# Performance work log

Hardware: AMD Instinct MI355X
Metric: run time of the kernel (lower is better)

Reference implementation:

```python
import jax, jax.numpy as jnp
import numpy as np
import math

B, S, D, H, DFF = 2, 2048, 1024, 16, 4096
DK = D // H
EPS = 1e-5


def setup_inputs() -> dict:
    key = jax.random.key(0)
    ks = jax.random.split(key, 8)
    s = 0.02
    return {
        "x": jax.random.normal(ks[0], (B, S, D), jnp.float32),
        "src_mask": jnp.ones((B, 1, 1, S), jnp.int32),
        "wq": jax.random.normal(ks[1], (D, D), jnp.float32) * s,
        "bq": jnp.zeros((D,), jnp.float32),
        "wk": jax.random.normal(ks[2], (D, D), jnp.float32) * s,
        "bk": jnp.zeros((D,), jnp.float32),
        "wv": jax.random.normal(ks[3], (D, D), jnp.float32) * s,
        "bv": jnp.zeros((D,), jnp.float32),
        "wo": jax.random.normal(ks[4], (D, D), jnp.float32) * s,
        "bo": jnp.zeros((D,), jnp.float32),
        "w1": jax.random.normal(ks[5], (DFF, D), jnp.float32) * s,
        "b1": jnp.zeros((DFF,), jnp.float32),
        "w2": jax.random.normal(ks[6], (D, DFF), jnp.float32) * s,
        "b2": jnp.zeros((D,), jnp.float32),
        "alpha1": jnp.ones((1,), jnp.float32),
        "bias1": jnp.ones((1,), jnp.float32),
        "alpha2": jnp.ones((1,), jnp.float32),
        "bias2": jnp.ones((1,), jnp.float32),
    }


def _layernorm(x, alpha, bias):
    # Faithful to source: unbiased std (ddof=1), divide by (std + eps),
    # scalar alpha/bias both initialized to 1.
    mean = jnp.mean(x, axis=-1, keepdims=True)
    std = jnp.std(x, axis=-1, keepdims=True, ddof=1)
    return alpha * (x - mean) / (std + EPS) + bias


def _mha(x, wq, bq, wk, bk, wv, bv, wo, bo):
    q = (x @ wq.T + bq).reshape(B, S, H, DK).swapaxes(1, 2)  # b h s d
    k = (x @ wk.T + bk).reshape(B, S, H, DK).swapaxes(1, 2)
    v = (x @ wv.T + bv).reshape(B, S, H, DK).swapaxes(1, 2)
    scores = jnp.einsum("bhqd,bhkd->bhqk", q, k) / math.sqrt(DK)
    # NOTE: source calls masked_fill (out-of-place) and discards the result,
    # so the mask has NO effect. Reproduced faithfully: no masking here.
    attn = jax.nn.softmax(scores, axis=-1)
    out = jnp.einsum("bhqk,bhkd->bhqd", attn, v)
    out = out.swapaxes(1, 2).reshape(B, S, D)
    return out @ wo.T + bo


def reference(x, src_mask, wq, bq, wk, bk, wv, bv, wo, bo,
              w1, b1, w2, b2, alpha1, bias1, alpha2, bias2):
    # residual[0]: x + attn(norm(x)) (dropout=0 -> identity)
    h1 = x + _mha(_layernorm(x, alpha1, bias1), wq, bq, wk, bk, wv, bv, wo, bo)
    # residual[1]: h1 + ffn(norm(h1))
    n2 = _layernorm(h1, alpha2, bias2)
    ffn = (n2 @ w1.T + b1) @ w2.T + b2
    return h1 + ffn
```

## Files before the change

### kernel.cpp

```cpp
#include <hip/hip_runtime.h>
#include <stdint.h>

#define Bx   2
#define Sx   2048
#define Dx   1024
#define Hx   16
#define DKx  64
#define DFFx 4096
#define Mx   4096

#define CEXP 0.18033688011112042f

typedef __attribute__((ext_vector_type(8))) short short8;
typedef __attribute__((ext_vector_type(4))) float f32x4;
typedef __attribute__((ext_vector_type(4))) unsigned short ushort4v;

__device__ __forceinline__ unsigned short f2b(float f) {
    union { float f; uint32_t u; } v; v.f = f;
    uint32_t u = v.u;
    u += 0x7fffu + ((u >> 16) & 1u);
    return (unsigned short)(u >> 16);
}

__device__ __forceinline__ float fexp2(float x) {
#if __has_builtin(__builtin_amdgcn_exp2f)
    return __builtin_amdgcn_exp2f(x);
#else
    return exp2f(x);
#endif
}

__global__ __launch_bounds__(256) void conv_all(
    const float4* __restrict__ wq, const float4* __restrict__ wk,
    const float4* __restrict__ wv, const float4* __restrict__ wo,
    const float4* __restrict__ w1, const float4* __restrict__ w2,
    const float4* __restrict__ bq, const float4* __restrict__ bk,
    const float4* __restrict__ bv,
    ushort4v* __restrict__ dqkv, ushort4v* __restrict__ dwo,
    ushort4v* __restrict__ d1, ushort4v* __restrict__ d2,
    float4* __restrict__ dbias) {
    const int i = blockIdx.x * 256 + threadIdx.x;
    const int S4 = 1 << 18;
    if (i < 4 * S4) {
        const float4* s; ushort4v* d;
        if (i < S4)          { s = wq + i;            d = dqkv + i; }
        else if (i < 2 * S4) { s = wk + (i - S4);     d = dqkv + i; }
        else if (i < 3 * S4) { s = wv + (i - 2 * S4); d = dqkv + i; }
        else                 { s = wo + (i - 3 * S4); d = dwo + (i - 3 * S4); }
        const float4 v = *s;
        ushort4v o; o.x = f2b(v.x); o.y = f2b(v.y); o.z = f2b(v.z); o.w = f2b(v.w);
        *d = o;
    } else if (i < 8 * S4) {
        const float4 v = w1[i - 4 * S4];
        ushort4v o; o.x = f2b(v.x); o.y = f2b(v.y); o.z = f2b(v.z); o.w = f2b(v.w);
        d1[i - 4 * S4] = o;
    } else if (i < 12 * S4) {
        const float4 v = w2[i - 8 * S4];
        ushort4v o; o.x = f2b(v.x); o.y = f2b(v.y); o.z = f2b(v.z); o.w = f2b(v.w);
        d2[i - 8 * S4] = o;
    } else if (i < 12 * S4 + 768) {
        const int jn = i - 12 * S4;
        dbias[jn] = (jn < 256) ? bq[jn] : (jn < 512 ? bk[jn - 256] : bv[jn - 512]);
    }
}

__global__ __launch_bounds__(256) void layernorm_k(const float* __restrict__ x,
                                                   const float* __restrict__ alpha,
                                                   const float* __restrict__ beta,
                                                   unsigned short* __restrict__ out) {
    __shared__ float red[8];
    const int row = blockIdx.x;
    const int t = threadIdx.x, lane = t & 63, w = t >> 6;
    float4 v = ((const float4*)(x + (size_t)row * Dx))[t];
    float s = v.x + v.y + v.z + v.w;
    float q = v.x*v.x + v.y*v.y + v.z*v.z + v.w*v.w;
#pragma unroll
    for (int off = 1; off < 64; off <<= 1) {
        s += __shfl_xor(s, off);
        q += __shfl_xor(q, off);
    }
    if (lane == 0) { red[w] = s; red[4 + w] = q; }
    __syncthreads();
    s = red[0] + red[1] + red[2] + red[3];
    q = red[4] + red[5] + red[6] + red[7];
    const float mean = s * (1.0f / Dx);
    float var = (q - (float)Dx * mean * mean) * (1.0f / (Dx - 1));
    var = fmaxf(var, 0.0f);
    const float inv = alpha[0] / (sqrtf(var) + 1e-5f);
    const float bb = beta[0];
    ushort4v o;
    o.x = f2b((v.x - mean) * inv + bb);
    o.y = f2b((v.y - mean) * inv + bb);
    o.z = f2b((v.z - mean) * inv + bb);
    o.w = f2b((v.w - mean) * inv + bb);
    *(ushort4v*)(out + (size_t)row * Dx + t * 4) = o;
}

#define GLDS(gp, lp) __builtin_amdgcn_global_load_lds( \
    (const __attribute__((address_space(1))) unsigned int*)(gp), \
    (__attribute__((address_space(3))) unsigned int*)(lp), 16, 0, 0)

#define STAGE(buf, kt) do {                                                     \
    const int k0_ = (kt) << 5;                                                  \
    _Pragma("unroll")                                                           \
    for (int i_ = 0; i_ < MB/2; ++i_) {                                         \
      const int ca_ = (MB==4) ? (w*2 + i_) : w;                                 \
      GLDS(A + (size_t)(bm + ca_*16 + srow)*K + k0_ + skc*8, &As[buf][ca_*512]);\
    }                                                                           \
    _Pragma("unroll")                                                           \
    for (int i_ = 0; i_ < 2; ++i_) {                                            \
      const int cb_ = w*2 + i_;                                                 \
      GLDS(W + (size_t)(bn + cb_*16 + srow)*K + k0_ + skc*8, &Bs[buf][cb_*512]);\
    }                                                                           \
  } while (0)

template<int BM>
__global__ __launch_bounds__(256) void gemm2(const short* __restrict__ A,
                                             const short* __restrict__ W,
                                             const float* __restrict__ bias,
                                             const float* __restrict__ res,
                                             float* __restrict__ Cout,
                                             int M, int N, int K) {
    constexpr int MB = BM / 32;
    __shared__ alignas(16) short As[2][BM * 32];
    __shared__ alignas(16) short Bs[2][128 * 32];
    const int t = threadIdx.x, lane = t & 63, w = t >> 6;
    const int bb = blockIdx.x, xcd = bb & 7, jj = bb >> 3;
    const int bn = (jj & 7) * 128;
    const int bm = (xcd * 8 + (jj >> 3)) * BM;
    const int wm = (w >> 1) * (BM / 2), wn = (w & 1) * 64;
    const int srow = lane >> 2, skc = lane & 3;

    f32x4 acc[MB][4] = {};
    const int nkt = K >> 5;

    STAGE(0, 0);
    __syncthreads();
    int cur = 0;
    for (int kt = 0; kt < nkt; ++kt) {
        if (kt + 1 < nkt) STAGE(cur ^ 1, kt + 1);
        const short* as = &As[cur][0];
        const short* bs = &Bs[cur][0];
        short8 af[MB], bfr[4];
#pragma unroll
        for (int mb = 0; mb < MB; ++mb)
            af[mb] = *(const short8*)&as[(wm + mb * 16 + (lane & 15)) * 32 + (lane >> 4) * 8];
#pragma unroll
        for (int nb = 0; nb < 4; ++nb)
            bfr[nb] = *(const short8*)&bs[(wn + nb * 16 + (lane & 15)) * 32 + (lane >> 4) * 8];
#pragma unroll
        for (int mb = 0; mb < MB; ++mb)
#pragma unroll
            for (int nb = 0; nb < 4; ++nb)
                acc[mb][nb] = __builtin_amdgcn_mfma_f32_16x16x32_bf16(af[mb], bfr[nb], acc[mb][nb], 0, 0, 0);
        __syncthreads();
        cur ^= 1;
    }

    const int r0 = (lane >> 4) * 4, c0 = lane & 15;
#pragma unroll
    for (int mb = 0; mb < MB; ++mb)
#pragma unroll
        for (int nb = 0; nb < 4; ++nb) {
            const int col = bn + wn + nb * 16 + c0;
            const float bv = bias[col];
            const int row0 = bm + wm + mb * 16 + r0;
#pragma unroll
            for (int r = 0; r < 4; ++r) {
                const size_t idx = (size_t)(row0 + r) * N + col;
                Cout[idx] = acc[mb][nb][r] + bv + res[idx];
            }
        }
}

template<int MODE>
__global__ __launch_bounds__(256) void gemm128(const short* __restrict__ A,
                                               const short* __restrict__ W,
                                               const float* __restrict__ bias,
                                               void* __restrict__ Cout,
                                               int N, int K,
                                               unsigned short* __restrict__ Qout,
                                               unsigned short* __restrict__ Kout,
                                               unsigned short* __restrict__ Vout) {
    constexpr int MB = 4;
    __shared__ alignas(16) short As[2][128 * 32];
    __shared__ alignas(16) short Bs[2][128 * 32];
    const int t = threadIdx.x, lane = t & 63, w = t >> 6;
    const int bb = blockIdx.x, bpx = gridDim.x >> 3;
    const int g = (bb & 7) * bpx + (bb >> 3);
    const int bn = (g >> 5) * 128;
    const int bm = (g & 31) * 128;
    const int wm = (w >> 1) * 64, wn = (w & 1) * 64;
    const int srow = lane >> 2, skc = lane & 3;

    f32x4 acc[MB][4] = {};
    const int nkt = K >> 5;

    STAGE(0, 0);
    __syncthreads();
    int cur = 0;
    for (int kt = 0; kt < nkt; ++kt) {
        if (kt + 1 < nkt) STAGE(cur ^ 1, kt + 1);
        const short* as = &As[cur][0];
        const short* bs = &Bs[cur][0];
        short8 af[MB], bfr[4];
#pragma unroll
        for (int mb = 0; mb < MB; ++mb)
            af[mb] = *(const short8*)&as[(wm + mb * 16 + (lane & 15)) * 32 + (lane >> 4) * 8];
#pragma unroll
        for (int nb = 0; nb < 4; ++nb)
            bfr[nb] = *(const short8*)&bs[(wn + nb * 16 + (lane & 15)) * 32 + (lane >> 4) * 8];
#pragma unroll
        for (int mb = 0; mb < MB; ++mb)
#pragma unroll
            for (int nb = 0; nb < 4; ++nb)
                acc[mb][nb] = __builtin_amdgcn_mfma_f32_16x16x32_bf16(af[mb], bfr[nb], acc[mb][nb], 0, 0, 0);
        __syncthreads();
        cur ^= 1;
    }

    const int r0 = (lane >> 4) * 4, c0 = lane & 15;
#pragma unroll
    for (int mb = 0; mb < MB; ++mb)
#pragma unroll
        for (int nb = 0; nb < 4; ++nb) {
            const int col = bn + wn + nb * 16 + c0;
            const float bv = bias[col];
            const int row0 = bm + wm + mb * 16 + r0;
            if (MODE == 0) {
#pragma unroll
                for (int r = 0; r < 4; ++r)
                    ((unsigned short*)Cout)[(size_t)(row0 + r) * N + col] = f2b(acc[mb][nb][r] + bv);
            } else {
                if (col < 1024) {
#pragma unroll
                    for (int r = 0; r < 4; ++r)
                        Qout[(size_t)(row0 + r) * 1024 + col] = f2b((acc[mb][nb][r] + bv) * CEXP);
                } else if (col < 2048) {
#pragma unroll
                    for (int r = 0; r < 4; ++r)
                        Kout[(size_t)(row0 + r) * 1024 + (col - 1024)] = f2b(acc[mb][nb][r] + bv);
                } else {
                    const int dk = col - 2048, hh = dk >> 6, dlo = dk & 63;
                    const int bbv = row0 >> 11, s0 = row0 & 2047;
                    const int vrow = (bbv * 16 + hh) * 64 + dlo;
                    ushort4v pv;
                    pv.x = f2b(acc[mb][nb][0] + bv);
                    pv.y = f2b(acc[mb][nb][1] + bv);
                    pv.z = f2b(acc[mb][nb][2] + bv);
                    pv.w = f2b(acc[mb][nb][3] + bv);
                    *(ushort4v*)&Vout[(size_t)vrow * Sx + s0] = pv;
                }
            }
        }
}

__global__ __launch_bounds__(256) void gemmsk(const short* __restrict__ A,
                                              const short* __restrict__ W,
                                              float* __restrict__ P0,
                                              float* __restrict__ P1,
                                              int K) {
    constexpr int MB = 4;
    __shared__ alignas(16) short As[2][128 * 32];
    __shared__ alignas(16) short Bs[2][128 * 32];
    const int t = threadIdx.x, lane = t & 63, w = t >> 6;
    const int bb = blockIdx.x, xcd = bb & 7, jj = bb >> 3;
    const int bn = (jj & 7) * 128;
    const int p = (xcd << 3) | (jj >> 3);
    const int bm = (p & 31) * 128;
    const int kz = p >> 5;
    float* __restrict__ P = kz ? P1 : P0;
    const int wm = (w >> 1) * 64, wn = (w & 1) * 64;
    const int srow = lane >> 2, skc = lane & 3;

    f32x4 acc[MB][4] = {};
    const int nkt = (K >> 1) >> 5;
    const int kbeg = kz * nkt;

    STAGE(0, kbeg);
    __syncthreads();
    int cur = 0;
    for (int kt = kbeg; kt < kbeg + nkt; ++kt) {
        if (kt + 1 < kbeg + nkt) STAGE(cur ^ 1, kt + 1);
        const short* as = &As[cur][0];
        const short* bs = &Bs[cur][0];
        short8 af[MB], bfr[4];
#pragma unroll
        for (int mb = 0; mb < MB; ++mb)
            af[mb] = *(const short8*)&as[(wm + mb * 16 + (lane & 15)) * 32 + (lane >> 4) * 8];
#pragma unroll
        for (int nb = 0; nb < 4; ++nb)
            bfr[nb] = *(const short8*)&bs[(wn + nb * 16 + (lane & 15)) * 32 + (lane >> 4) * 8];
#pragma unroll
        for (int mb = 0; mb < MB; ++mb)
#pragma unroll
            for (int nb = 0; nb < 4; ++nb)
                acc[mb][nb] = __builtin_amdgcn_mfma_f32_16x16x32_bf16(af[mb], bfr[nb], acc[mb][nb], 0, 0, 0);
        __syncthreads();
        cur ^= 1;
    }

    const int r0 = (lane >> 4) * 4, c0 = lane & 15;
#pragma unroll
    for (int mb = 0; mb < MB; ++mb)
#pragma unroll
        for (int nb = 0; nb < 4; ++nb) {
            const int col = bn + wn + nb * 16 + c0;
            const int row0 = bm + wm + mb * 16 + r0;
#pragma unroll
            for (int r = 0; r < 4; ++r)
                P[(size_t)(row0 + r) * Dx + col] = acc[mb][nb][r];
        }
}

__global__ __launch_bounds__(256) void epi2(const float4* __restrict__ p0,
                                            const float4* __restrict__ p1,
                                            const float4* __restrict__ b2,
                                            const float4* __restrict__ h1,
                                            float4* __restrict__ out) {
    const int i = blockIdx.x * 256 + threadIdx.x;
    const float4 bv = b2[i & 255];
    const float4 a = p0[i], b = p1[i], h = h1[i];
    float4 o;
    o.x = a.x + b.x + h.x + bv.x;
    o.y = a.y + b.y + h.y + bv.y;
    o.z = a.z + b.z + h.z + bv.z;
    o.w = a.w + b.w + h.w + bv.w;
    out[i] = o;
}

__global__ __launch_bounds__(256) void attn_fwd6(const short* __restrict__ Q,
                                                 const short* __restrict__ Kg,
                                                 const short* __restrict__ Vtg,
                                                 unsigned short* __restrict__ O) {
    __shared__ alignas(16) short Ks[2][64 * 64];
    __shared__ alignas(16) short Vs[2][64 * 64];
    __shared__ alignas(16) short Pl[4][32 * 64];
    const int t = threadIdx.x, lane = t & 63, w = t >> 6;
    const int bh = blockIdx.x;
    const int b = bh >> 4, h = bh & 15;
    const int q0 = blockIdx.y * 128 + w * 32;
    const int lo = lane & 15, hi = lane >> 4;

    short8 qf[2][2];
#pragma unroll
    for (int mb = 0; mb < 2; ++mb)
#pragma unroll
        for (int kf = 0; kf < 2; ++kf)
            qf[mb][kf] = *(const short8*)&Q[(size_t)(b * Sx + q0 + mb * 16 + lo) * Dx
                                            + h * DKx + kf * 32 + hi * 8];

    f32x4 o_[2][4] = {};
    f32x4 l_acc[2] = {};
    short8 ones;
#pragma unroll
    for (int j = 0; j < 8; ++j) ones[j] = (short)0x3F80;

    const int srow = t >> 2;
    const int scol2 = (t & 3) * 32;
    const int swz = (srow & 7) << 4;
    const short* Kbase = Kg + (size_t)(b * Sx) * Dx + h * DKx;
    const short* Vbase = Vtg + (size_t)(bh * 64 + srow) * Sx;
    char* PwB = (char*)&Pl[w][0];

    short8 kr0, kr1, vr0, vr1;
    {
        const short* kp = Kbase + (size_t)srow * Dx + (t & 3) * 16;
        kr0 = *(const short8*)kp; kr1 = *(const short8*)(kp + 8);
        const short* vp = Vbase + (t & 3) * 16;
        vr0 = *(const short8*)vp; vr1 = *(const short8*)(vp + 8);
        char* KsB = (char*)&Ks[0][0];
        char* VsB = (char*)&Vs[0][0];
        *(short8*)(KsB + ((srow * 128 + scol2) ^ swz)) = kr0;
        *(short8*)(KsB + ((srow * 128 + scol2 + 16) ^ swz)) = kr1;
        *(short8*)(VsB + ((srow * 128 + scol2) ^ swz)) = vr0;
        *(short8*)(VsB + ((srow * 128 + scol2 + 16) ^ swz)) = vr1;
    }
    __syncthreads();

    int cur = 0;
    for (int kt = 0; kt < Sx / 64; ++kt) {
        const bool more = (kt + 1 < Sx / 64);
        if (more) {
            const short* kp = Kbase + (size_t)((kt + 1) * 64 + srow) * Dx + (t & 3) * 16;
            kr0 = *(const short8*)kp; kr1 = *(const short8*)(kp + 8);
            const short* vp = Vbase + (kt + 1) * 64 + (t & 3) * 16;
            vr0 = *(const short8*)vp; vr1 = *(const short8*)(vp + 8);
        }
        char* KsB = (char*)&Ks[cur][0];
        char* VsB = (char*)&Vs[cur][0];

        f32x4 s[2][4] = {};
        __builtin_amdgcn_s_setprio(1);
#pragma unroll
        for (int nb = 0; nb < 4; ++nb) {
            const int key = nb * 16 + lo;
            const int ksw = (key & 7) << 4;
#pragma unroll
            for (int kf = 0; kf < 2; ++kf) {
                const short8 kfr = *(const short8*)(KsB + ((key * 128 + kf * 64 + hi * 16) ^ ksw));
#pragma unroll
                for (int mb = 0; mb < 2; ++mb)
                    s[mb][nb] = __builtin_amdgcn_mfma_f32_16x16x32_bf16(qf[mb][kf], kfr, s[mb][nb], 0, 0, 0);
            }
        }
        __builtin_amdgcn_s_setprio(0);

#pragma unroll
        for (int mb = 0; mb < 2; ++mb)
#pragma unroll
            for (int nb = 0; nb < 4; ++nb) {
                const int k = nb * 16 + lo;
#pragma unroll
                for (int r = 0; r < 4; ++r) {
                    const float p = fexp2(s[mb][nb][r]);
                    union { float f; uint32_t u; } cv; cv.f = p;
                    const int qq = mb * 16 + hi * 4 + r;
                    *(short*)(PwB + ((qq * 128 + k * 2) ^ ((qq & 7) << 4))) = (short)(cv.u >> 16);
                }
            }

        short8 pa[2][2];
#pragma unroll
        for (int mb = 0; mb < 2; ++mb)
#pragma unroll
            for (int kc = 0; kc < 2; ++kc)
                pa[mb][kc] = *(const short8*)(PwB + (((mb * 16 + lo) * 128 + kc * 64 + hi * 16) ^ ((lo & 7) << 4)));

        __builtin_amdgcn_s_setprio(1);
#pragma unroll
        for (int mb = 0; mb < 2; ++mb) {
            l_acc[mb] = __builtin_amdgcn_mfma_f32_16x16x32_bf16(pa[mb][0], ones, l_acc[mb], 0, 0, 0);
            l_acc[mb] = __builtin_amdgcn_mfma_f32_16x16x32_bf16(pa[mb][1], ones, l_acc[mb], 0, 0, 0);
        }

#pragma unroll
        for (int d = 0; d < 4; ++d) {
            const int vd = d * 16 + lo;
            const int vsw = (vd & 7) << 4;
#pragma unroll
            for (int kc = 0; kc < 2; ++kc) {
                const short8 vf = *(const short8*)(VsB + ((vd * 128 + kc * 64 + hi * 16) ^ vsw));
#pragma unroll
                for (int mb = 0; mb < 2; ++mb)
                    o_[mb][d] = __builtin_amdgcn_mfma_f32_16x16x32_bf16(pa[mb][kc], vf, o_[mb][d], 0, 0, 0);
            }
        }
        __builtin_amdgcn_s_setprio(0);

        if (more) {
            char* KsN = (char*)&Ks[cur ^ 1][0];
            char* VsN = (char*)&Vs[cur ^ 1][0];
            *(short8*)(KsN + ((srow * 128 + scol2) ^ swz)) = kr0;
            *(short8*)(KsN + ((srow * 128 + scol2 + 16) ^ swz)) = kr1;
            *(short8*)(VsN + ((srow * 128 + scol2) ^ swz)) = vr0;
            *(short8*)(VsN + ((srow * 128 + scol2 + 16) ^ swz)) = vr1;
        }
        __syncthreads();
        cur ^= 1;
    }

#pragma unroll
    for (int mb = 0; mb < 2; ++mb)
#pragma unroll
        for (int d = 0; d < 4; ++d)
#pragma unroll
            for (int r = 0; r < 4; ++r) {
                const int qrow = b * Sx + q0 + mb * 16 + hi * 4 + r;
                O[(size_t)qrow * Dx + h * DKx + d * 16 + lo] = f2b(o_[mb][d][r] / l_acc[mb][r]);
            }
}

extern "C" void kernel_launch(void* const* d_in, const int* in_sizes, int n_in,
                              void* d_out, int out_size, void* d_ws, size_t ws_size,
                              hipStream_t stream) {
    const float* x  = (const float*)d_in[0];
    const float* wq = (const float*)d_in[2];
    const float* bq = (const float*)d_in[3];
    const float* wk = (const float*)d_in[4];
    const float* bk = (const float*)d_in[5];
    const float* wv = (const float*)d_in[6];
    const float* bv = (const float*)d_in[7];
    const float* wo = (const float*)d_in[8];
    const float* bo = (const float*)d_in[9];
    const float* w1 = (const float*)d_in[10];
    const float* b1 = (const float*)d_in[11];
    const float* w2 = (const float*)d_in[12];
    const float* b2 = (const float*)d_in[13];
    const float* alpha1 = (const float*)d_in[14];
    const float* bias1  = (const float*)d_in[15];
    const float* alpha2 = (const float*)d_in[16];
    const float* bias2  = (const float*)d_in[17];
    float* out = (float*)d_out;

    short* ws   = (short*)d_ws;
    short* wqkv = ws;
    short* wob  = wqkv + 3145728;
    short* w1b  = wob  + 1048576;
    short* w2b  = w1b  + 4194304;
    short* n1   = w2b  + 4194304;
    short* Qb   = n1   + 4194304;
    short* Kb   = Qb   + 4194304;
    short* Vt   = Kb   + 4194304;
    short* f1   = Vt   + 4194304;
    float* h1   = (float*)(f1 + 16777216);
    float* bqkv = (float*)((char*)h1 + ((size_t)Mx * Dx * 4));
    short* ao = n1;
    short* n2 = n1;
    float* p0 = (float*)n1;
    float* p1 = (float*)Kb;

    conv_all<<<12291, 256, 0, stream>>>((const float4*)wq, (const float4*)wk,
                                        (const float4*)wv, (const float4*)wo,
                                        (const float4*)w1, (const float4*)w2,
                                        (const float4*)bq, (const float4*)bk,
                                        (const float4*)bv,
                                        (ushort4v*)wqkv, (ushort4v*)wob,
                                        (ushort4v*)w1b, (ushort4v*)w2b,
                                        (float4*)bqkv);

    layernorm_k<<<Mx, 256, 0, stream>>>(x, alpha1, bias1, (unsigned short*)n1);

    gemm128<2><<<768, 256, 0, stream>>>(n1, wqkv, bqkv, nullptr, 3072, Dx,
                                        (unsigned short*)Qb, (unsigned short*)Kb,
                                        (unsigned short*)Vt);

    attn_fwd6<<<dim3(32, 16), 256, 0, stream>>>(Qb, Kb, Vt, (unsigned short*)ao);

    gemm2<64><<<512, 256, 0, stream>>>(ao, wob, bo, x, h1, Mx, Dx, Dx);

    layernorm_k<<<Mx, 256, 0, stream>>>(h1, alpha2, bias2, (unsigned short*)n2);

    gemm128<0><<<1024, 256, 0, stream>>>(n2, w1b, b1, f1, DFFx, Dx,
                                         nullptr, nullptr, nullptr);

    gemmsk<<<512, 256, 0, stream>>>(f1, w2b, p0, p1, DFFx);
    epi2<<<4096, 256, 0, stream>>>((const float4*)p0, (const float4*)p1,
                                   (const float4*)b2, (const float4*)h1, (float4*)out);
}
```

Baseline: 361.6 us.

## Use 256x256 tiles with 512 threads for QKV and FFN1 GEMMs, transpose MFMA operands

Replaces the 128x128 gemm128 kernel with a gemm256 kernel that computes 256x256 output tiles using 8 waves, which doubles operand reuse per LDS load and lowers global traffic per FLOP. Across all GEMMs the MFMA operand order is swapped so each lane holds four consecutive columns, which allows vectorized float4/ushort4 epilogue stores. The trade-offs are higher register pressure (32 accumulators per wave) and fewer blocks (192/256) on the device. The V-transpose output also goes from one packed store to four scalar stores.

```diff
diff --git a/kernel.cpp b/kernel.cpp
--- a/kernel.cpp
+++ b/kernel.cpp
@@ -125,6 +125,7 @@
     __shared__ alignas(16) short As[2][BM * 32];
     __shared__ alignas(16) short Bs[2][128 * 32];
     const int t = threadIdx.x, lane = t & 63, w = t >> 6;
+    const int lo = lane & 15, hi = lane >> 4;
     const int bb = blockIdx.x, xcd = bb & 7, jj = bb >> 3;
     const int bn = (jj & 7) * 128;
     const int bm = (xcd * 8 + (jj >> 3)) * BM;
@@ -144,112 +145,136 @@
         short8 af[MB], bfr[4];
 #pragma unroll
         for (int mb = 0; mb < MB; ++mb)
-            af[mb] = *(const short8*)&as[(wm + mb * 16 + (lane & 15)) * 32 + (lane >> 4) * 8];
+            af[mb] = *(const short8*)&as[(wm + mb * 16 + lo) * 32 + hi * 8];
 #pragma unroll
         for (int nb = 0; nb < 4; ++nb)
-            bfr[nb] = *(const short8*)&bs[(wn + nb * 16 + (lane & 15)) * 32 + (lane >> 4) * 8];
+            bfr[nb] = *(const short8*)&bs[(wn + nb * 16 + lo) * 32 + hi * 8];
 #pragma unroll
         for (int mb = 0; mb < MB; ++mb)
 #pragma unroll
             for (int nb = 0; nb < 4; ++nb)
-                acc[mb][nb] = __builtin_amdgcn_mfma_f32_16x16x32_bf16(af[mb], bfr[nb], acc[mb][nb], 0, 0, 0);
+                acc[mb][nb] = __builtin_amdgcn_mfma_f32_16x16x32_bf16(bfr[nb], af[mb], acc[mb][nb], 0, 0, 0);
         __syncthreads();
         cur ^= 1;
     }
 
-    const int r0 = (lane >> 4) * 4, c0 = lane & 15;
 #pragma unroll
     for (int mb = 0; mb < MB; ++mb)
 #pragma unroll
         for (int nb = 0; nb < 4; ++nb) {
-            const int col = bn + wn + nb * 16 + c0;
-            const float bv = bias[col];
-            const int row0 = bm + wm + mb * 16 + r0;
-#pragma unroll
-            for (int r = 0; r < 4; ++r) {
-                const size_t idx = (size_t)(row0 + r) * N + col;
-                Cout[idx] = acc[mb][nb][r] + bv + res[idx];
-            }
-        }
-}
+            const int row = bm + wm + mb * 16 + lo;
+            const int col0 = bn + wn + nb * 16 + hi * 4;
+            const float4 bv4 = *(const float4*)&bias[col0];
+            const size_t idx = (size_t)row * N + col0;
+            const float4 rs4 = *(const float4*)&res[idx];
+            float4 o4;
+            o4.x = acc[mb][nb][0] + bv4.x + rs4.x;
+            o4.y = acc[mb][nb][1] + bv4.y + rs4.y;
+            o4.z = acc[mb][nb][2] + bv4.z + rs4.z;
+            o4.w = acc[mb][nb][3] + bv4.w + rs4.w;
+            *(float4*)&Cout[idx] = o4;
+        }
+}
+
+#define STG256(buf, kt) do {                                                     \
+    const int k0_ = (kt) << 5;                                                   \
+    _Pragma("unroll")                                                            \
+    for (int i_ = 0; i_ < 2; ++i_) {                                             \
+      const int c_ = i_ * 8 + w;                                                 \
+      GLDS(A + (size_t)(bm + c_*16 + (lane>>2))*K + k0_ + (lane&3)*8,            \
+           &As[buf][c_*512]);                                                    \
+      GLDS(W + (size_t)(bn + c_*16 + (lane>>2))*K + k0_ + (lane&3)*8,            \
+           &Bs[buf][c_*512]);                                                    \
+    }                                                                            \
+  } while (0)
 
 template<int MODE>
-__global__ __launch_bounds__(256) void gemm128(const short* __restrict__ A,
-                                               const short* __restrict__ W,
-                                               const float* __restrict__ bias,
-                                               void* __restrict__ Cout,
-                                               int N, int K,
-                                               unsigned short* __restrict__ Qout,
-                                               unsigned short* __restrict__ Kout,
-                                               unsigned short* __restrict__ Vout) {
-    constexpr int MB = 4;
-    __shared__ alignas(16) short As[2][128 * 32];
-    __shared__ alignas(16) short Bs[2][128 * 32];
+__global__ __launch_bounds__(512, 2) void gemm256(const short* __restrict__ A,
+                                                  const short* __restrict__ W,
+                                                  const float* __restrict__ bias,
+                                                  void* __restrict__ Cout,
+                                                  int M, int N, int K,
+                                                  int nbn, int rpx,
+                                                  unsigned short* __restrict__ Qout,
+                                                  unsigned short* __restrict__ Kout,
+                                                  unsigned short* __restrict__ Vout) {
+    __shared__ alignas(16) short As[2][256 * 32];
+    __shared__ alignas(16) short Bs[2][256 * 32];
     const int t = threadIdx.x, lane = t & 63, w = t >> 6;
-    const int bb = blockIdx.x, bpx = gridDim.x >> 3;
-    const int g = (bb & 7) * bpx + (bb >> 3);
-    const int bn = (g >> 5) * 128;
-    const int bm = (g & 31) * 128;
-    const int wm = (w >> 1) * 64, wn = (w & 1) * 64;
-    const int srow = lane >> 2, skc = lane & 3;
-
-    f32x4 acc[MB][4] = {};
+    const int lo = lane & 15, hi = lane >> 4;
+    const int bb = blockIdx.x, xcd = bb & 7, jj = bb >> 3;
+    const int bm = (xcd * rpx + jj / nbn) * 256;
+    const int bn = (jj % nbn) * 256;
+    const int wr = w >> 2, wc = w & 3;
+
+    f32x4 acc[8][4] = {};
     const int nkt = K >> 5;
 
-    STAGE(0, 0);
+    STG256(0, 0);
     __syncthreads();
     int cur = 0;
     for (int kt = 0; kt < nkt; ++kt) {
-        if (kt + 1 < nkt) STAGE(cur ^ 1, kt + 1);
+        if (kt + 1 < nkt) STG256(cur ^ 1, kt + 1);
         const short* as = &As[cur][0];
         const short* bs = &Bs[cur][0];
-        short8 af[MB], bfr[4];
-#pragma unroll
-        for (int mb = 0; mb < MB; ++mb)
-            af[mb] = *(const short8*)&as[(wm + mb * 16 + (lane & 15)) * 32 + (lane >> 4) * 8];
+        short8 bfr[4];
 #pragma unroll
         for (int nb = 0; nb < 4; ++nb)
-            bfr[nb] = *(const short8*)&bs[(wn + nb * 16 + (lane & 15)) * 32 + (lane >> 4) * 8];
-#pragma unroll
-        for (int mb = 0; mb < MB; ++mb)
-#pragma unroll
-            for (int nb = 0; nb < 4; ++nb)
-                acc[mb][nb] = __builtin_amdgcn_mfma_f32_16x16x32_bf16(af[mb], bfr[nb], acc[mb][nb], 0, 0, 0);
+            bfr[nb] = *(const short8*)&bs[(wc * 64 + nb * 16 + lo) * 32 + hi * 8];
+#pragma unroll
+        for (int mh = 0; mh < 2; ++mh) {
+            short8 af[4];
+#pragma unroll
+            for (int mb = 0; mb < 4; ++mb)
+                af[mb] = *(const short8*)&as[(wr * 128 + mh * 64 + mb * 16 + lo) * 32 + hi * 8];
+#pragma unroll
+            for (int mb = 0; mb < 4; ++mb)
+#pragma unroll
+                for (int nb = 0; nb < 4; ++nb)
+                    acc[mh * 4 + mb][nb] =
+                        __builtin_amdgcn_mfma_f32_16x16x32_bf16(bfr[nb], af[mb], acc[mh * 4 + mb][nb], 0, 0, 0);
+        }
         __syncthreads();
         cur ^= 1;
     }
 
-    const int r0 = (lane >> 4) * 4, c0 = lane & 15;
-#pragma unroll
-    for (int mb = 0; mb < MB; ++mb)
+#pragma unroll
+    for (int mb = 0; mb < 8; ++mb)
 #pragma unroll
         for (int nb = 0; nb < 4; ++nb) {
-            const int col = bn + wn + nb * 16 + c0;
-            const float bv = bias[col];
-            const int row0 = bm + wm + mb * 16 + r0;
+            const int row = bm + wr * 128 + mb * 16 + lo;
+            const int col0 = bn + wc * 64 + nb * 16 + hi * 4;
+            const float4 bv4 = *(const float4*)&bias[col0];
             if (MODE == 0) {
-#pragma unroll
-                for (int r = 0; r < 4; ++r)
-                    ((unsigned short*)Cout)[(size_t)(row0 + r) * N + col] = f2b(acc[mb][nb][r] + bv);
+                ushort4v pv;
+                pv.x = f2b(acc[mb][nb][0] + bv4.x);
+                pv.y = f2b(acc[mb][nb][1] + bv4.y);
+                pv.z = f2b(acc[mb][nb][2] + bv4.z);
+                pv.w = f2b(acc[mb][nb][3] + bv4.w);
+                *(ushort4v*)&((unsigned short*)Cout)[(size_t)row * N + col0] = pv;
             } else {
-                if (col < 1024) {
-#pragma unroll
-                    for (int r = 0; r < 4; ++r)
-                        Qout[(size_t)(row0 + r) * 1024 + col] = f2b((acc[mb][nb][r] + bv) * CEXP);
-                } else if (col < 2048) {
-#pragma unroll
-                    for (int r = 0; r < 4; ++r)
-                        Kout[(size_t)(row0 + r) * 1024 + (col - 1024)] = f2b(acc[mb][nb][r] + bv);
+                if (col0 < 1024) {
+                    ushort4v pv;
+                    pv.x = f2b((acc[mb][nb][0] + bv4.x) * CEXP);
+                    pv.y = f2b((acc[mb][nb][1] + bv4.y) * CEXP);
+                    pv.z = f2b((acc[mb][nb][2] + bv4.z) * CEXP);
+                    pv.w = f2b((acc[mb][nb][3] + bv4.w) * CEXP);
+                    *(ushort4v*)&Qout[(size_t)row * 1024 + col0] = pv;
+                } else if (col0 < 2048) {
+                    ushort4v pv;
+                    pv.x = f2b(acc[mb][nb][0] + bv4.x);
+                    pv.y = f2b(acc[mb][nb][1] + bv4.y);
+                    pv.z = f2b(acc[mb][nb][2] + bv4.z);
+                    pv.w = f2b(acc[mb][nb][3] + bv4.w);
+                    *(ushort4v*)&Kout[(size_t)row * 1024 + (col0 - 1024)] = pv;
                 } else {
-                    const int dk = col - 2048, hh = dk >> 6, dlo = dk & 63;
-                    const int bbv = row0 >> 11, s0 = row0 & 2047;
-                    const int vrow = (bbv * 16 + hh) * 64 + dlo;
-                    ushort4v pv;
-                    pv.x = f2b(acc[mb][nb][0] + bv);
-                    pv.y = f2b(acc[mb][nb][1] + bv);
-                    pv.z = f2b(acc[mb][nb][2] + bv);
-                    pv.w = f2b(acc[mb][nb][3] + bv);
-                    *(ushort4v*)&Vout[(size_t)vrow * Sx + s0] = pv;
+                    const int bbv = row >> 11, s0 = row & 2047;
+#pragma unroll
+                    for (int j = 0; j < 4; ++j) {
+                        const int dk = col0 - 2048 + j;
+                        const int vrow = (bbv * 16 + (dk >> 6)) * 64 + (dk & 63);
+                        Vout[(size_t)vrow * Sx + s0] = f2b(acc[mb][nb][j] + ((const float*)&bv4)[j]);
+                    }
                 }
             }
         }
@@ -264,6 +289,7 @@
     __shared__ alignas(16) short As[2][128 * 32];
     __shared__ alignas(16) short Bs[2][128 * 32];
     const int t = threadIdx.x, lane = t & 63, w = t >> 6;
+    const int lo = lane & 15, hi = lane >> 4;
     const int bb = blockIdx.x, xcd = bb & 7, jj = bb >> 3;
     const int bn = (jj & 7) * 128;
     const int p = (xcd << 3) | (jj >> 3);
@@ -287,29 +313,29 @@
         short8 af[MB], bfr[4];
 #pragma unroll
         for (int mb = 0; mb < MB; ++mb)
-            af[mb] = *(const short8*)&as[(wm + mb * 16 + (lane & 15)) * 32 + (lane >> 4) * 8];
+            af[mb] = *(const short8*)&as[(wm + mb * 16 + lo) * 32 + hi * 8];
 #pragma unroll
         for (int nb = 0; nb < 4; ++nb)
-            bfr[nb] = *(const short8*)&bs[(wn + nb * 16 + (lane & 15)) * 32 + (lane >> 4) * 8];
+            bfr[nb] = *(const short8*)&bs[(wn + nb * 16 + lo) * 32 + hi * 8];
 #pragma unroll
         for (int mb = 0; mb < MB; ++mb)
 #pragma unroll
             for (int nb = 0; nb < 4; ++nb)
-                acc[mb][nb] = __builtin_amdgcn_mfma_f32_16x16x32_bf16(af[mb], bfr[nb], acc[mb][nb], 0, 0, 0);
+                acc[mb][nb] = __builtin_amdgcn_mfma_f32_16x16x32_bf16(bfr[nb], af[mb], acc[mb][nb], 0, 0, 0);
         __syncthreads();
         cur ^= 1;
     }
 
-    const int r0 = (lane >> 4) * 4, c0 = lane & 15;
 #pragma unroll
     for (int mb = 0; mb < MB; ++mb)
 #pragma unroll
         for (int nb = 0; nb < 4; ++nb) {
-            const int col = bn + wn + nb * 16 + c0;
-            const int row0 = bm + wm + mb * 16 + r0;
-#pragma unroll
-            for (int r = 0; r < 4; ++r)
-                P[(size_t)(row0 + r) * Dx + col] = acc[mb][nb][r];
+            const int row = bm + wm + mb * 16 + lo;
+            const int col0 = bn + wn + nb * 16 + hi * 4;
+            float4 o4;
+            o4.x = acc[mb][nb][0]; o4.y = acc[mb][nb][1];
+            o4.z = acc[mb][nb][2]; o4.w = acc[mb][nb][3];
+            *(float4*)&P[(size_t)row * Dx + col0] = o4;
         }
 }
 
@@ -521,7 +547,8 @@
 
     layernorm_k<<<Mx, 256, 0, stream>>>(x, alpha1, bias1, (unsigned short*)n1);
 
-    gemm128<2><<<768, 256, 0, stream>>>(n1, wqkv, bqkv, nullptr, 3072, Dx,
+    gemm256<2><<<192, 512, 0, stream>>>(n1, wqkv, bqkv, nullptr,
+                                        Mx, 3072, Dx, 12, 2,
                                         (unsigned short*)Qb, (unsigned short*)Kb,
                                         (unsigned short*)Vt);
 
@@ -531,8 +558,8 @@
 
     layernorm_k<<<Mx, 256, 0, stream>>>(h1, alpha2, bias2, (unsigned short*)n2);
 
-    gemm128<0><<<1024, 256, 0, stream>>>(n2, w1b, b1, f1, DFFx, Dx,
-                                         nullptr, nullptr, nullptr);
+    gemm256<0><<<256, 512, 0, stream>>>(n2, w1b, b1, f1,
+                                        Mx, DFFx, Dx, 16, 2, nullptr, nullptr, nullptr);
 
     gemmsk<<<512, 256, 0, stream>>>(f1, w2b, p0, p1, DFFx);
     epi2<<<4096, 256, 0, stream>>>((const float4*)p0, (const float4*)p1,
```

New measurement: 378.0 us. 4.5% more time.
